# Performance work log

Hardware: AMD Instinct MI355X
Metric: run time of the kernel (lower is better)

Reference implementation:

```python
import jax, jax.numpy as jnp
import numpy as np

B, S, D, H = 2, 2048, 1024, 16
HS = D // H  # head size 64
EPS = 1e-5


def setup_inputs() -> dict:
    key = jax.random.key(0)
    ks = jax.random.split(key, 12)
    s = lambda fan_in: 1.0 / np.sqrt(fan_in)
    return {
        "x": jax.random.normal(ks[0], (B, S, D), dtype=jnp.float32),
        # per-head QKV weights, math orientation [H, D, HS] (x @ W)
        "wq": jax.random.normal(ks[1], (H, D, HS), dtype=jnp.float32) * s(D),
        "wk": jax.random.normal(ks[2], (H, D, HS), dtype=jnp.float32) * s(D),
        "wv": jax.random.normal(ks[3], (H, D, HS), dtype=jnp.float32) * s(D),
        "wproj": jax.random.normal(ks[4], (D, D), dtype=jnp.float32) * s(D),
        "bproj": jnp.zeros((D,), dtype=jnp.float32),
        "w1": jax.random.normal(ks[5], (D, 4 * D), dtype=jnp.float32) * s(D),
        "b1": jnp.zeros((4 * D,), dtype=jnp.float32),
        "w2": jax.random.normal(ks[6], (4 * D, D), dtype=jnp.float32) * s(4 * D),
        "b2": jnp.zeros((D,), dtype=jnp.float32),
        "ln1_g": jnp.ones((D,), dtype=jnp.float32),
        "ln1_b": jnp.zeros((D,), dtype=jnp.float32),
        "ln2_g": jnp.ones((D,), dtype=jnp.float32),
        "ln2_b": jnp.zeros((D,), dtype=jnp.float32),
    }


def _layernorm(x, g, b):
    mu = jnp.mean(x, axis=-1, keepdims=True)
    var = jnp.mean(jnp.square(x - mu), axis=-1, keepdims=True)
    return (x - mu) * jax.lax.rsqrt(var + EPS) * g + b


def reference(x, wq, wk, wv, wproj, bproj, w1, b1, w2, b2, ln1_g, ln1_b, ln2_g, ln2_b):
    Bq, T, C = x.shape
    xn = _layernorm(x, ln1_g, ln1_b)
    # per-head projections, batched over heads
    q = jnp.einsum('btd,hdk->bhtk', xn, wq)
    k = jnp.einsum('btd,hdk->bhtk', xn, wk)
    v = jnp.einsum('btd,hdk->bhtk', xn, wv)
    scale = k.shape[-1] ** (-0.5)
    scores = jnp.einsum('bhtk,bhsk->bhts', q, k) * scale  # [B,H,T,T]
    causal = jnp.tril(jnp.ones((T, T), dtype=bool))
    scores = jnp.where(causal, scores, -jnp.inf)
    att = jax.nn.softmax(scores, axis=-1)
    out = jnp.einsum('bhts,bhsk->bhtk', att, v)  # [B,H,T,HS]
    out = out.transpose(0, 2, 1, 3).reshape(Bq, T, C)  # concat heads
    attn_out = out @ wproj + bproj
    h = x + attn_out
    hn = _layernorm(h, ln2_g, ln2_b)
    ff = jax.nn.relu(hn @ w1 + b1) @ w2 + b2
    return h + ff
```

## Files before the change

kernel.cpp:

```cpp
#include <hip/hip_runtime.h>


typedef __bf16 bf16_t;
typedef __attribute__((ext_vector_type(8))) __bf16 bf16x8;
typedef __attribute__((ext_vector_type(4))) __bf16 bf16x4;
typedef __attribute__((ext_vector_type(4))) float f32x4;

__device__ __forceinline__ f32x4 mfma16(bf16x8 a, bf16x8 b, f32x4 c) {
  return __builtin_amdgcn_mfma_f32_16x16x32_bf16(a, b, c, 0, 0, 0);
}

__device__ __forceinline__ void gll16(const void* g, void* l) {
  __builtin_amdgcn_global_load_lds(
      (const __attribute__((address_space(1))) void*)g,
      (__attribute__((address_space(3))) void*)l, 16, 0, 0);
}

__global__ __launch_bounds__(256) void ln_kernel(
    const float* __restrict__ x, const float* __restrict__ g,
    const float* __restrict__ be, bf16_t* __restrict__ out) {
  const int row = blockIdx.x;
  const int tid = threadIdx.x;
  const float4 v = *(reinterpret_cast<const float4*>(x + (size_t)row * 1024) + tid);
  float s1 = v.x + v.y + v.z + v.w;
  float s2 = v.x * v.x + v.y * v.y + v.z * v.z + v.w * v.w;
#pragma unroll
  for (int off = 1; off < 64; off <<= 1) {
    s1 += __shfl_xor(s1, off);
    s2 += __shfl_xor(s2, off);
  }
  __shared__ float red[8];
  const int l = tid & 63, w = tid >> 6;
  if (l == 0) { red[w] = s1; red[w + 4] = s2; }
  __syncthreads();
  s1 = red[0] + red[1] + red[2] + red[3];
  s2 = red[4] + red[5] + red[6] + red[7];
  const float mu = s1 * (1.f / 1024.f);
  const float var = s2 * (1.f / 1024.f) - mu * mu;
  const float rstd = rsqrtf(var + 1e-5f);
  const float4 gg = *(reinterpret_cast<const float4*>(g) + tid);
  const float4 bb = *(reinterpret_cast<const float4*>(be) + tid);
  bf16x4 o;
  o[0] = (bf16_t)((v.x - mu) * rstd * gg.x + bb.x);
  o[1] = (bf16_t)((v.y - mu) * rstd * gg.y + bb.y);
  o[2] = (bf16_t)((v.z - mu) * rstd * gg.z + bb.z);
  o[3] = (bf16_t)((v.w - mu) * rstd * gg.w + bb.w);
  *(reinterpret_cast<bf16x4*>(out + (size_t)row * 1024) + tid) = o;
}

__global__ __launch_bounds__(256) void transpose_cvt(
    const float* __restrict__ in, bf16_t* __restrict__ out, int R, int C) {
  __shared__ float t[32][33];
  const int bz = blockIdx.z;
  in += (size_t)bz * R * C;
  out += (size_t)bz * R * C;
  const int c0 = blockIdx.x * 32, r0 = blockIdx.y * 32;
  const int tx = threadIdx.x, ty = threadIdx.y;
#pragma unroll
  for (int i = 0; i < 4; i++)
    t[ty + i * 8][tx] = in[(size_t)(r0 + ty + i * 8) * C + c0 + tx];
  __syncthreads();
#pragma unroll
  for (int i = 0; i < 4; i++)
    out[(size_t)(c0 + ty + i * 8) * R + r0 + tx] = (bf16_t)t[tx][ty + i * 8];
}

template <int MODE>
__global__ __launch_bounds__(256) void gemm_bt(
    const bf16_t* __restrict__ A, const bf16_t* __restrict__ BT,
    const float* __restrict__ bias, const float* __restrict__ resid,
    void* __restrict__ out0, void* __restrict__ out1, int M, int N, int K) {
  __shared__ __align__(16) bf16_t Al[128 * 32];
  __shared__ __align__(16) bf16_t Bl[128 * 32];
  const int tid = threadIdx.x;
  const int l = tid & 63, w = tid >> 6;
  const int wr = w >> 1, wc = w & 1;
  const int lr = l & 15, lg = l >> 4;
  const int bm = blockIdx.y * 128, bn = blockIdx.x * 128;

  f32x4 acc[4][4];
#pragma unroll
  for (int i = 0; i < 4; i++)
#pragma unroll
    for (int j = 0; j < 4; j++) acc[i][j] = (f32x4)(0.f);

  const char* Ag = (const char*)(A + (size_t)bm * K);
  const char* Bg = (const char*)(BT + (size_t)bn * K);
  const size_t rowb = (size_t)K * 2;
  const int nK = K >> 5;

  for (int kt = 0; kt < nK; ++kt) {
#pragma unroll
    for (int i = 0; i < 2; i++) {
      const int s = i * 256 + tid;
      const size_t go = (size_t)(s >> 2) * rowb + (size_t)(kt * 64 + (s & 3) * 16);
      gll16(Ag + go, (char*)Al + (i * 256 + w * 64) * 16);
      gll16(Bg + go, (char*)Bl + (i * 256 + w * 64) * 16);
    }
    __syncthreads();
    bf16x8 af[4], bfr[4];
#pragma unroll
    for (int mi = 0; mi < 4; mi++)
      af[mi] = *reinterpret_cast<const bf16x8*>(Al + (wr * 64 + mi * 16 + lr) * 32 + lg * 8);
#pragma unroll
    for (int ni = 0; ni < 4; ni++)
      bfr[ni] = *reinterpret_cast<const bf16x8*>(Bl + (wc * 64 + ni * 16 + lr) * 32 + lg * 8);
#pragma unroll
    for (int mi = 0; mi < 4; mi++)
#pragma unroll
      for (int ni = 0; ni < 4; ni++)
        acc[mi][ni] = mfma16(af[mi], bfr[ni], acc[mi][ni]);
    __syncthreads();
  }

#pragma unroll
  for (int mi = 0; mi < 4; mi++) {
    const int r = bm + wr * 64 + mi * 16 + lg * 4;
#pragma unroll
    for (int ni = 0; ni < 4; ni++) {
      const int c = bn + wc * 64 + ni * 16 + lr;
      f32x4 v = acc[mi][ni];
      if constexpr (MODE == 1) {
        const float bb = bias[c];
        float* o = (float*)out0;
#pragma unroll
        for (int j = 0; j < 4; j++)
          o[(size_t)(r + j) * N + c] = v[j] + bb + resid[(size_t)(r + j) * N + c];
      } else if constexpr (MODE == 2) {
        const float bb = bias[c];
        bf16_t* o = (bf16_t*)out0;
#pragma unroll
        for (int j = 0; j < 4; j++)
          o[(size_t)(r + j) * N + c] = (bf16_t)fmaxf(v[j] + bb, 0.f);
      } else {
        if (c < 2048) {
          bf16_t* o = (bf16_t*)out0;
#pragma unroll
          for (int j = 0; j < 4; j++)
            o[(size_t)(r + j) * 2048 + c] = (bf16_t)v[j];
        } else {
          const int nn = c - 2048;
          const int bI = r >> 11, tl = r & 2047;
          bf16x4 pk;
#pragma unroll
          for (int j = 0; j < 4; j++) pk[j] = (bf16_t)v[j];
          *reinterpret_cast<bf16x4*>((bf16_t*)out1 +
              ((size_t)(bI * 1024 + nn)) * 2048 + tl) = pk;
        }
      }
    }
  }
}

__global__ __launch_bounds__(256) void attn_kernel(
    const bf16_t* __restrict__ qk, const bf16_t* __restrict__ vT,
    bf16_t* __restrict__ ac) {
  const int qt = blockIdx.x;
  const int bh = blockIdx.y;
  const int b = bh >> 4, h = bh & 15;
  const int tid = threadIdx.x;
  const int l = tid & 63, w = tid >> 6;
  const int lr = l & 15, lg = l >> 4;

  __shared__ __align__(16) bf16_t kl[64 * 72];
  __shared__ __align__(16) bf16_t vl[64 * 72];
  __shared__ __align__(16) bf16_t pl[4][16 * 72];

  const bf16_t* qp = qk + ((size_t)(b * 2048 + qt * 64 + w * 16 + lr)) * 2048 + h * 64;
  bf16x8 qf[2];
  qf[0] = *reinterpret_cast<const bf16x8*>(qp + lg * 8);
  qf[1] = *reinterpret_cast<const bf16x8*>(qp + 32 + lg * 8);

  f32x4 oacc[4];
#pragma unroll
  for (int i = 0; i < 4; i++) oacc[i] = (f32x4)(0.f);
  float mrow[4], lrow[4];
#pragma unroll
  for (int j = 0; j < 4; j++) { mrow[j] = -1e30f; lrow[j] = 0.f; }
  const int rbase = qt * 64 + w * 16 + lg * 4;

  for (int st = 0; st <= qt; ++st) {
    __syncthreads();
#pragma unroll
    for (int i = 0; i < 2; i++) {
      const int ch = tid + i * 256;
      const int r = ch >> 3, c = (ch & 7) * 8;
      *reinterpret_cast<bf16x8*>(&kl[r * 72 + c]) =
          *reinterpret_cast<const bf16x8*>(
              qk + ((size_t)(b * 2048 + st * 64 + r)) * 2048 + 1024 + h * 64 + c);
      *reinterpret_cast<bf16x8*>(&vl[r * 72 + c]) =
          *reinterpret_cast<const bf16x8*>(
              vT + ((size_t)(bh * 64 + r)) * 2048 + st * 64 + c);
    }
    __syncthreads();

    f32x4 sc4[4];
#pragma unroll
    for (int ct = 0; ct < 4; ct++) sc4[ct] = (f32x4)(0.f);
#pragma unroll
    for (int ct = 0; ct < 4; ct++)
#pragma unroll
      for (int kc = 0; kc < 2; kc++) {
        bf16x8 kf = *reinterpret_cast<const bf16x8*>(
            &kl[(ct * 16 + lr) * 72 + kc * 32 + lg * 8]);
        sc4[ct] = mfma16(qf[kc], kf, sc4[ct]);
      }

#pragma unroll
    for (int ct = 0; ct < 4; ct++)
#pragma unroll
      for (int j = 0; j < 4; j++) {
        float sv = sc4[ct][j] * 0.125f;
        if (st == qt) {
          const int col = st * 64 + ct * 16 + lr;
          if (col > rbase + j) sv = -1e30f;
        }
        sc4[ct][j] = sv;
      }

    float rmax[4];
#pragma unroll
    for (int j = 0; j < 4; j++)
      rmax[j] = fmaxf(fmaxf(sc4[0][j], sc4[1][j]), fmaxf(sc4[2][j], sc4[3][j]));
#pragma unroll
    for (int off = 1; off < 16; off <<= 1)
#pragma unroll
      for (int j = 0; j < 4; j++) rmax[j] = fmaxf(rmax[j], __shfl_xor(rmax[j], off));
    float fac[4];
#pragma unroll
    for (int j = 0; j < 4; j++) {
      const float mn = fmaxf(mrow[j], rmax[j]);
      fac[j] = __expf(mrow[j] - mn);
      mrow[j] = mn;
    }
    float rsum[4] = {0.f, 0.f, 0.f, 0.f};
#pragma unroll
    for (int ct = 0; ct < 4; ct++)
#pragma unroll
      for (int j = 0; j < 4; j++) {
        const float p = __expf(sc4[ct][j] - mrow[j]);
        sc4[ct][j] = p;
        rsum[j] += p;
      }
#pragma unroll
    for (int off = 1; off < 16; off <<= 1)
#pragma unroll
      for (int j = 0; j < 4; j++) rsum[j] += __shfl_xor(rsum[j], off);
#pragma unroll
    for (int j = 0; j < 4; j++) lrow[j] = lrow[j] * fac[j] + rsum[j];
#pragma unroll
    for (int ht = 0; ht < 4; ht++)
#pragma unroll
      for (int j = 0; j < 4; j++) oacc[ht][j] *= fac[j];

#pragma unroll
    for (int ct = 0; ct < 4; ct++)
#pragma unroll
      for (int j = 0; j < 4; j++)
        pl[w][(lg * 4 + j) * 72 + ct * 16 + lr] = (bf16_t)sc4[ct][j];
    bf16x8 pf[2];
#pragma unroll
    for (int sc = 0; sc < 2; sc++)
      pf[sc] = *reinterpret_cast<const bf16x8*>(&pl[w][lr * 72 + sc * 32 + lg * 8]);

#pragma unroll
    for (int ht = 0; ht < 4; ht++)
#pragma unroll
      for (int sc = 0; sc < 2; sc++) {
        bf16x8 vf = *reinterpret_cast<const bf16x8*>(
            &vl[(ht * 16 + lr) * 72 + sc * 32 + lg * 8]);
        oacc[ht] = mfma16(pf[sc], vf, oacc[ht]);
      }
  }

#pragma unroll
  for (int ht = 0; ht < 4; ht++)
#pragma unroll
    for (int j = 0; j < 4; j++) {
      const size_t t = (size_t)(b * 2048 + qt * 64 + w * 16 + lg * 4 + j);
      ac[t * 1024 + h * 64 + ht * 16 + lr] = (bf16_t)(oacc[ht][j] / lrow[j]);
    }
}

extern "C" void kernel_launch(void* const* d_in, const int* in_sizes, int n_in,
                              void* d_out, int out_size, void* d_ws, size_t ws_size,
                              hipStream_t stream) {
  const float* x     = (const float*)d_in[0];
  const float* wq    = (const float*)d_in[1];
  const float* wk    = (const float*)d_in[2];
  const float* wv    = (const float*)d_in[3];
  const float* wproj = (const float*)d_in[4];
  const float* bproj = (const float*)d_in[5];
  const float* w1    = (const float*)d_in[6];
  const float* b1    = (const float*)d_in[7];
  const float* w2    = (const float*)d_in[8];
  const float* b2    = (const float*)d_in[9];
  const float* ln1g  = (const float*)d_in[10];
  const float* ln1b  = (const float*)d_in[11];
  const float* ln2g  = (const float*)d_in[12];
  const float* ln2b  = (const float*)d_in[13];
  float* out = (float*)d_out;

  char* ws = (char*)d_ws;
  const size_t MB = 1 << 20;
  bf16_t* xn  = (bf16_t*)(ws + 0);
  bf16_t* wT  = (bf16_t*)(ws + 8 * MB);
  float*  hbuf= (float*)(ws + 16 * MB);
  bf16_t* qkb = (bf16_t*)(ws + 32 * MB);
  bf16_t* vTb = (bf16_t*)(ws + 48 * MB);
  bf16_t* acb = (bf16_t*)(ws + 56 * MB);
  bf16_t* ffa = (bf16_t*)(ws + 32 * MB);
  bf16_t* hn  = xn;

  dim3 tb(32, 8);

  ln_kernel<<<4096, 256, 0, stream>>>(x, ln1g, ln1b, xn);
  transpose_cvt<<<dim3(2, 32, 16), tb, 0, stream>>>(wq, wT, 1024, 64);
  transpose_cvt<<<dim3(2, 32, 16), tb, 0, stream>>>(wk, wT + 1024 * 1024, 1024, 64);
  transpose_cvt<<<dim3(2, 32, 16), tb, 0, stream>>>(wv, wT + 2048 * 1024, 1024, 64);
  gemm_bt<0><<<dim3(24, 32), 256, 0, stream>>>(xn, wT, nullptr, nullptr, qkb, vTb,
                                               4096, 3072, 1024);
  attn_kernel<<<dim3(32, 32), 256, 0, stream>>>(qkb, vTb, acb);
  transpose_cvt<<<dim3(32, 32, 1), tb, 0, stream>>>(wproj, wT, 1024, 1024);
  gemm_bt<1><<<dim3(8, 32), 256, 0, stream>>>(acb, wT, bproj, x, hbuf, nullptr,
                                              4096, 1024, 1024);
  ln_kernel<<<4096, 256, 0, stream>>>(hbuf, ln2g, ln2b, hn);
  transpose_cvt<<<dim3(128, 32, 1), tb, 0, stream>>>(w1, wT, 1024, 4096);
  gemm_bt<2><<<dim3(32, 32), 256, 0, stream>>>(hn, wT, b1, nullptr, ffa, nullptr,
                                               4096, 4096, 1024);
  transpose_cvt<<<dim3(32, 128, 1), tb, 0, stream>>>(w2, wT, 4096, 1024);
  gemm_bt<1><<<dim3(8, 32), 256, 0, stream>>>(ffa, wT, b2, hbuf, out, nullptr,
                                              4096, 1024, 4096);
}
```

Before: 468.7 us.

## Pair causal query tiles per block, prefetch K/V, and swizzle GEMM blocks

The attention kernel now gives each block a pair of query tiles (p and 31-p) for the same head, so every block does an equal amount of causal work, and each K/V tile loaded into LDS is shared by both tiles. The next K/V tile is prefetched into registers while the current one is computed, hiding global load latency. The GEMM remaps block indices in an XCD-aware round-robin (stride 8) to improve L2 locality. The changes cost more registers for the doubled accumulators and halve the attention grid to 512 blocks.

```diff
diff --git a/kernel.cpp b/kernel.cpp
--- a/kernel.cpp
+++ b/kernel.cpp
@@ -76,7 +76,11 @@
   const int l = tid & 63, w = tid >> 6;
   const int wr = w >> 1, wc = w & 1;
   const int lr = l & 15, lg = l >> 4;
-  const int bm = blockIdx.y * 128, bn = blockIdx.x * 128;
+  const int gx = gridDim.x;
+  const int nwg = gx * gridDim.y;
+  int flat = blockIdx.y * gx + blockIdx.x;
+  flat = (flat & 7) * (nwg >> 3) + (flat >> 3);
+  const int bm = (flat / gx) * 128, bn = (flat % gx) * 128;
 
   f32x4 acc[4][4];
 #pragma unroll
@@ -152,11 +156,90 @@
   }
 }
 
+__device__ __forceinline__ void attn_tile(
+    const bf16_t* __restrict__ kl, const bf16_t* __restrict__ vl,
+    bf16_t* __restrict__ plw, const bf16x8* qf, f32x4* oacc,
+    float* mrow, float* lrow, const int lr, const int lg,
+    const int rbase, const int cbase, const bool diag) {
+  f32x4 sc4[4];
+#pragma unroll
+  for (int ct = 0; ct < 4; ct++) sc4[ct] = (f32x4)(0.f);
+#pragma unroll
+  for (int ct = 0; ct < 4; ct++)
+#pragma unroll
+    for (int kc = 0; kc < 2; kc++) {
+      bf16x8 kf = *reinterpret_cast<const bf16x8*>(
+          &kl[(ct * 16 + lr) * 72 + kc * 32 + lg * 8]);
+      sc4[ct] = mfma16(qf[kc], kf, sc4[ct]);
+    }
+#pragma unroll
+  for (int ct = 0; ct < 4; ct++)
+#pragma unroll
+    for (int j = 0; j < 4; j++) {
+      float sv = sc4[ct][j] * 0.125f;
+      if (diag && (cbase + ct * 16 + lr > rbase + j)) sv = -1e30f;
+      sc4[ct][j] = sv;
+    }
+  float rmax[4];
+#pragma unroll
+  for (int j = 0; j < 4; j++)
+    rmax[j] = fmaxf(fmaxf(sc4[0][j], sc4[1][j]), fmaxf(sc4[2][j], sc4[3][j]));
+#pragma unroll
+  for (int off = 1; off < 16; off <<= 1)
+#pragma unroll
+    for (int j = 0; j < 4; j++) rmax[j] = fmaxf(rmax[j], __shfl_xor(rmax[j], off));
+  float fac[4];
+#pragma unroll
+  for (int j = 0; j < 4; j++) {
+    const float mn = fmaxf(mrow[j], rmax[j]);
+    fac[j] = __expf(mrow[j] - mn);
+    mrow[j] = mn;
+  }
+  float rsum[4] = {0.f, 0.f, 0.f, 0.f};
+#pragma unroll
+  for (int ct = 0; ct < 4; ct++)
+#pragma unroll
+    for (int j = 0; j < 4; j++) {
+      const float pv = __expf(sc4[ct][j] - mrow[j]);
+      sc4[ct][j] = pv;
+      rsum[j] += pv;
+    }
+#pragma unroll
+  for (int off = 1; off < 16; off <<= 1)
+#pragma unroll
+    for (int j = 0; j < 4; j++) rsum[j] += __shfl_xor(rsum[j], off);
+#pragma unroll
+  for (int j = 0; j < 4; j++) lrow[j] = lrow[j] * fac[j] + rsum[j];
+#pragma unroll
+  for (int ht = 0; ht < 4; ht++)
+#pragma unroll
+    for (int j = 0; j < 4; j++) oacc[ht][j] *= fac[j];
+#pragma unroll
+  for (int ct = 0; ct < 4; ct++)
+#pragma unroll
+    for (int j = 0; j < 4; j++)
+      plw[(lg * 4 + j) * 72 + ct * 16 + lr] = (bf16_t)sc4[ct][j];
+  bf16x8 pf[2];
+#pragma unroll
+  for (int sc = 0; sc < 2; sc++)
+    pf[sc] = *reinterpret_cast<const bf16x8*>(&plw[lr * 72 + sc * 32 + lg * 8]);
+#pragma unroll
+  for (int ht = 0; ht < 4; ht++)
+#pragma unroll
+    for (int sc = 0; sc < 2; sc++) {
+      bf16x8 vf = *reinterpret_cast<const bf16x8*>(
+          &vl[(ht * 16 + lr) * 72 + sc * 32 + lg * 8]);
+      oacc[ht] = mfma16(pf[sc], vf, oacc[ht]);
+    }
+}
+
 __global__ __launch_bounds__(256) void attn_kernel(
     const bf16_t* __restrict__ qk, const bf16_t* __restrict__ vT,
     bf16_t* __restrict__ ac) {
-  const int qt = blockIdx.x;
-  const int bh = blockIdx.y;
+  const int f = blockIdx.x;
+  const int bh = (f & 7) + 8 * ((f >> 3) & 3);
+  const int p = f >> 5;
+  const int qlo = p, qhi = 31 - p;
   const int b = bh >> 4, h = bh & 15;
   const int tid = threadIdx.x;
   const int l = tid & 63, w = tid >> 6;
@@ -165,120 +248,69 @@
   __shared__ __align__(16) bf16_t kl[64 * 72];
   __shared__ __align__(16) bf16_t vl[64 * 72];
   __shared__ __align__(16) bf16_t pl[4][16 * 72];
-
-  const bf16_t* qp = qk + ((size_t)(b * 2048 + qt * 64 + w * 16 + lr)) * 2048 + h * 64;
-  bf16x8 qf[2];
-  qf[0] = *reinterpret_cast<const bf16x8*>(qp + lg * 8);
-  qf[1] = *reinterpret_cast<const bf16x8*>(qp + 32 + lg * 8);
-
-  f32x4 oacc[4];
-#pragma unroll
-  for (int i = 0; i < 4; i++) oacc[i] = (f32x4)(0.f);
-  float mrow[4], lrow[4];
-#pragma unroll
-  for (int j = 0; j < 4; j++) { mrow[j] = -1e30f; lrow[j] = 0.f; }
-  const int rbase = qt * 64 + w * 16 + lg * 4;
-
-  for (int st = 0; st <= qt; ++st) {
+  bf16_t* plw = pl[w];
+
+  const bf16_t* qb = qk + ((size_t)(b * 2048 + w * 16 + lr)) * 2048 + h * 64;
+  bf16x8 qfl[2], qfh[2];
+#pragma unroll
+  for (int kc = 0; kc < 2; kc++) {
+    qfl[kc] = *(const bf16x8*)(qb + (size_t)qlo * 64 * 2048 + kc * 32 + lg * 8);
+    qfh[kc] = *(const bf16x8*)(qb + (size_t)qhi * 64 * 2048 + kc * 32 + lg * 8);
+  }
+
+  f32x4 oaccl[4], oacch[4];
+  float ml[4], llo[4], mh[4], lhi[4];
+#pragma unroll
+  for (int i = 0; i < 4; i++) { oaccl[i] = (f32x4)(0.f); oacch[i] = (f32x4)(0.f); }
+#pragma unroll
+  for (int j = 0; j < 4; j++) { ml[j] = -1e30f; llo[j] = 0.f; mh[j] = -1e30f; lhi[j] = 0.f; }
+
+  const int rlo = qlo * 64 + w * 16 + lg * 4;
+  const int rhi = qhi * 64 + w * 16 + lg * 4;
+
+  const int r0 = tid >> 3, c0 = (tid & 7) * 8;
+  const bf16_t* kg = qk + ((size_t)(b * 2048)) * 2048 + 1024 + h * 64;
+  const bf16_t* vg = vT + ((size_t)(bh * 64)) * 2048;
+
+  bf16x8 kreg[2], vreg[2];
+#pragma unroll
+  for (int i = 0; i < 2; i++) {
+    const int r = r0 + i * 32;
+    kreg[i] = *(const bf16x8*)(kg + (size_t)r * 2048 + c0);
+    vreg[i] = *(const bf16x8*)(vg + (size_t)r * 2048 + c0);
+  }
+
+  const int nst = qhi + 1;
+  for (int st = 0; st < nst; ++st) {
     __syncthreads();
 #pragma unroll
     for (int i = 0; i < 2; i++) {
-      const int ch = tid + i * 256;
-      const int r = ch >> 3, c = (ch & 7) * 8;
-      *reinterpret_cast<bf16x8*>(&kl[r * 72 + c]) =
-          *reinterpret_cast<const bf16x8*>(
-              qk + ((size_t)(b * 2048 + st * 64 + r)) * 2048 + 1024 + h * 64 + c);
-      *reinterpret_cast<bf16x8*>(&vl[r * 72 + c]) =
-          *reinterpret_cast<const bf16x8*>(
-              vT + ((size_t)(bh * 64 + r)) * 2048 + st * 64 + c);
+      const int r = r0 + i * 32;
+      *(bf16x8*)(&kl[r * 72 + c0]) = kreg[i];
+      *(bf16x8*)(&vl[r * 72 + c0]) = vreg[i];
     }
     __syncthreads();
-
-    f32x4 sc4[4];
-#pragma unroll
-    for (int ct = 0; ct < 4; ct++) sc4[ct] = (f32x4)(0.f);
-#pragma unroll
-    for (int ct = 0; ct < 4; ct++)
-#pragma unroll
-      for (int kc = 0; kc < 2; kc++) {
-        bf16x8 kf = *reinterpret_cast<const bf16x8*>(
-            &kl[(ct * 16 + lr) * 72 + kc * 32 + lg * 8]);
-        sc4[ct] = mfma16(qf[kc], kf, sc4[ct]);
+    if (st + 1 < nst) {
+#pragma unroll
+      for (int i = 0; i < 2; i++) {
+        const int r = r0 + i * 32;
+        kreg[i] = *(const bf16x8*)(kg + (size_t)((st + 1) * 64 + r) * 2048 + c0);
+        vreg[i] = *(const bf16x8*)(vg + (size_t)r * 2048 + (st + 1) * 64 + c0);
       }
-
-#pragma unroll
-    for (int ct = 0; ct < 4; ct++)
-#pragma unroll
-      for (int j = 0; j < 4; j++) {
-        float sv = sc4[ct][j] * 0.125f;
-        if (st == qt) {
-          const int col = st * 64 + ct * 16 + lr;
-          if (col > rbase + j) sv = -1e30f;
-        }
-        sc4[ct][j] = sv;
-      }
-
-    float rmax[4];
-#pragma unroll
-    for (int j = 0; j < 4; j++)
-      rmax[j] = fmaxf(fmaxf(sc4[0][j], sc4[1][j]), fmaxf(sc4[2][j], sc4[3][j]));
-#pragma unroll
-    for (int off = 1; off < 16; off <<= 1)
-#pragma unroll
-      for (int j = 0; j < 4; j++) rmax[j] = fmaxf(rmax[j], __shfl_xor(rmax[j], off));
-    float fac[4];
+    }
+    attn_tile(kl, vl, plw, qfh, oacch, mh, lhi, lr, lg, rhi, st * 64, st == qhi);
+    if (st <= qlo)
+      attn_tile(kl, vl, plw, qfl, oaccl, ml, llo, lr, lg, rlo, st * 64, st == qlo);
+  }
+
+#pragma unroll
+  for (int ht = 0; ht < 4; ht++)
 #pragma unroll
     for (int j = 0; j < 4; j++) {
-      const float mn = fmaxf(mrow[j], rmax[j]);
-      fac[j] = __expf(mrow[j] - mn);
-      mrow[j] = mn;
-    }
-    float rsum[4] = {0.f, 0.f, 0.f, 0.f};
-#pragma unroll
-    for (int ct = 0; ct < 4; ct++)
-#pragma unroll
-      for (int j = 0; j < 4; j++) {
-        const float p = __expf(sc4[ct][j] - mrow[j]);
-        sc4[ct][j] = p;
-        rsum[j] += p;
-      }
-#pragma unroll
-    for (int off = 1; off < 16; off <<= 1)
-#pragma unroll
-      for (int j = 0; j < 4; j++) rsum[j] += __shfl_xor(rsum[j], off);
-#pragma unroll
-    for (int j = 0; j < 4; j++) lrow[j] = lrow[j] * fac[j] + rsum[j];
-#pragma unroll
-    for (int ht = 0; ht < 4; ht++)
-#pragma unroll
-      for (int j = 0; j < 4; j++) oacc[ht][j] *= fac[j];
-
-#pragma unroll
-    for (int ct = 0; ct < 4; ct++)
-#pragma unroll
-      for (int j = 0; j < 4; j++)
-        pl[w][(lg * 4 + j) * 72 + ct * 16 + lr] = (bf16_t)sc4[ct][j];
-    bf16x8 pf[2];
-#pragma unroll
-    for (int sc = 0; sc < 2; sc++)
-      pf[sc] = *reinterpret_cast<const bf16x8*>(&pl[w][lr * 72 + sc * 32 + lg * 8]);
-
-#pragma unroll
-    for (int ht = 0; ht < 4; ht++)
-#pragma unroll
-      for (int sc = 0; sc < 2; sc++) {
-        bf16x8 vf = *reinterpret_cast<const bf16x8*>(
-            &vl[(ht * 16 + lr) * 72 + sc * 32 + lg * 8]);
-        oacc[ht] = mfma16(pf[sc], vf, oacc[ht]);
-      }
-  }
-
-#pragma unroll
-  for (int ht = 0; ht < 4; ht++)
-#pragma unroll
-    for (int j = 0; j < 4; j++) {
-      const size_t t = (size_t)(b * 2048 + qt * 64 + w * 16 + lg * 4 + j);
-      ac[t * 1024 + h * 64 + ht * 16 + lr] = (bf16_t)(oacc[ht][j] / lrow[j]);
+      const size_t tl = (size_t)(b * 2048 + rlo + j);
+      ac[tl * 1024 + h * 64 + ht * 16 + lr] = (bf16_t)(oaccl[ht][j] / llo[j]);
+      const size_t th = (size_t)(b * 2048 + rhi + j);
+      ac[th * 1024 + h * 64 + ht * 16 + lr] = (bf16_t)(oacch[ht][j] / lhi[j]);
     }
 }
 
@@ -320,7 +352,7 @@
   transpose_cvt<<<dim3(2, 32, 16), tb, 0, stream>>>(wv, wT + 2048 * 1024, 1024, 64);
   gemm_bt<0><<<dim3(24, 32), 256, 0, stream>>>(xn, wT, nullptr, nullptr, qkb, vTb,
                                                4096, 3072, 1024);
-  attn_kernel<<<dim3(32, 32), 256, 0, stream>>>(qkb, vTb, acb);
+  attn_kernel<<<512, 256, 0, stream>>>(qkb, vTb, acb);
   transpose_cvt<<<dim3(32, 32, 1), tb, 0, stream>>>(wproj, wT, 1024, 1024);
   gemm_bt<1><<<dim3(8, 32), 256, 0, stream>>>(acb, wT, bproj, x, hbuf, nullptr,
                                               4096, 1024, 1024);
```

After: 425.9 us. 1.1x faster.
